# Kernel tuning notes

Hardware: AMD Instinct MI355X
Metric: run time of the kernel (lower is better)

The kernel has to match this reference:

```python
import jax, jax.numpy as jnp
import numpy as np

N_JOINTS = 50
N_BONES = 50  # mask slicing [:, :, :50] / [:, :, :150] in the source requires exactly 50 bones
# Original repo's getSkeletalModelStructure() is not provided; use deterministic
# bone pairs (i, (i+1) % 50) over the 50 joints. Same gather+norm+direction math.
BONE_A = np.arange(N_JOINTS)
BONE_B = (BONE_A + 1) % N_JOINTS


def _length_direct(x):
    # x: [B, T, 150] -> joints [B, T, 50, 3]
    B, T, _ = x.shape
    joints = x.reshape(B, T, N_JOINTS, 3)
    diff = joints[:, :, BONE_A, :] - joints[:, :, BONE_B, :]  # [B, T, 50, 3]
    length = jnp.linalg.norm(diff, axis=-1)                   # [B, T, 50]
    tiny = jnp.finfo(x.dtype).tiny
    direct = diff / (length[..., None] + tiny)                # [B, T, 50, 3]
    return length, direct.reshape(B, T, N_BONES * 3)          # [B, T, 150]


def setup_inputs() -> dict:
    key = jax.random.key(0)
    k1, k2 = jax.random.split(key)
    shape = (128, 1024, 150)
    return {
        "preds": jax.random.normal(k1, shape, dtype=jnp.float32),
        "targets": jax.random.normal(k2, shape, dtype=jnp.float32),
    }


def reference(preds, targets):
    target_pad = 0.0
    loss_scale = 0.1
    mask = (targets != target_pad).astype(preds.dtype)  # [B, T, 150]
    p = preds * mask
    t = targets * mask
    # lengths are computed in the original but unused in the final loss;
    # only the direction terms enter the bone loss.
    _, p_dir = _length_direct(p)
    _, t_dir = _length_direct(t)
    p_dir = p_dir * mask[:, :, :150]
    t_dir = t_dir * mask[:, :, :150]
    loss = jnp.mean(jnp.abs(p - t)) + 0.1 * jnp.mean((p_dir - t_dir) ** 2)
    return loss * loss_scale
```

## Files before the change

kernel.cpp:

```cpp
#include <hip/hip_runtime.h>

constexpr int      FRAMES  = 128 * 1024;
constexpr int      FRAME_F = 150;
constexpr unsigned NT      = (unsigned)FRAMES * 50u;
constexpr unsigned NC      = NT / 4u;
constexpr float    SCALE   = 0.1f / ((float)FRAMES * (float)FRAME_F);

constexpr int      BLOCK   = 256;
constexpr int      NBLK    = 2048;
constexpr unsigned G       = (unsigned)NBLK * BLOCK;

__device__ __forceinline__ float bone_term(
    float p0, float p1, float p2, float t0, float t1, float t2,
    float q0, float q1, float q2, float u0, float u1, float u2)
{
    const float m0 = (t0 != 0.0f) ? 1.0f : 0.0f;
    const float m1 = (t1 != 0.0f) ? 1.0f : 0.0f;
    const float m2 = (t2 != 0.0f) ? 1.0f : 0.0f;
    const float n0 = (u0 != 0.0f) ? 1.0f : 0.0f;
    const float n1 = (u1 != 0.0f) ? 1.0f : 0.0f;
    const float n2 = (u2 != 0.0f) ? 1.0f : 0.0f;

    const float pm0 = p0 * m0, pm1 = p1 * m1, pm2 = p2 * m2;
    const float qm0 = q0 * n0, qm1 = q1 * n1, qm2 = q2 * n2;

    const float ab = fabsf(pm0 - t0) + fabsf(pm1 - t1) + fabsf(pm2 - t2);

    const float pd0 = pm0 - qm0, pd1 = pm1 - qm1, pd2 = pm2 - qm2;
    const float td0 = t0 - u0,   td1 = t1 - u1,   td2 = t2 - u2;

    const float pl2 = pd0*pd0 + pd1*pd1 + pd2*pd2;
    const float tl2 = td0*td0 + td1*td1 + td2*td2;
    const float pri = (pl2 > 0.0f) ? __builtin_amdgcn_rsqf(pl2) : 0.0f;
    const float tri = (tl2 > 0.0f) ? __builtin_amdgcn_rsqf(tl2) : 0.0f;

    const float d0 = pd0 * pri - td0 * tri;
    const float d1 = pd1 * pri - td1 * tri;
    const float d2 = pd2 * pri - td2 * tri;
    const float sq = m0*d0*d0 + m1*d1*d1 + m2*d2*d2;

    return ab + 0.1f * sq;
}

__global__ __launch_bounds__(BLOCK, 4) void bone_loss_main(
    const float* __restrict__ preds,
    const float* __restrict__ targets,
    float* __restrict__ partials)
{
    const unsigned tid = blockIdx.x * BLOCK + threadIdx.x;
    float acc = 0.0f;

    #pragma clang loop unroll(disable)
    for (unsigned c = tid; c < NC; c += G) {
        const unsigned bt = c * 4u;
        const unsigned j0 = bt % 50u;
        const float* P = preds   + (size_t)bt * 3u;
        const float* T = targets + (size_t)bt * 3u;

        const bool w1 = (j0 == 48u);
        const bool w3 = (j0 == 46u);
        const int eoff = w3 ? 0 : 12;
        const int woff = w1 ? -144 : (w3 ? -138 : 0);

        const float4 pa = *reinterpret_cast<const float4*>(P + 0);
        const float4 pb = *reinterpret_cast<const float4*>(P + 4);
        const float4 pc = *reinterpret_cast<const float4*>(P + 8);
        const float4 ps = *reinterpret_cast<const float4*>(P + eoff);
        const float4 ta = *reinterpret_cast<const float4*>(T + 0);
        const float4 tb = *reinterpret_cast<const float4*>(T + 4);
        const float4 tc = *reinterpret_cast<const float4*>(T + 8);
        const float4 ts = *reinterpret_cast<const float4*>(T + eoff);
        const float pw0 = P[woff+0], pw1 = P[woff+1], pw2 = P[woff+2];
        const float tw0 = T[woff+0], tw1 = T[woff+1], tw2 = T[woff+2];

        acc += bone_term(pa.x, pa.y, pa.z,  ta.x, ta.y, ta.z,
                         pa.w, pb.x, pb.y,  ta.w, tb.x, tb.y);
        acc += bone_term(pa.w, pb.x, pb.y,  ta.w, tb.x, tb.y,
                         w1 ? pw0 : pb.z, w1 ? pw1 : pb.w, w1 ? pw2 : pc.x,
                         w1 ? tw0 : tb.z, w1 ? tw1 : tb.w, w1 ? tw2 : tc.x);
        acc += bone_term(pb.z, pb.w, pc.x,  tb.z, tb.w, tc.x,
                         pc.y, pc.z, pc.w,  tc.y, tc.z, tc.w);
        acc += bone_term(pc.y, pc.z, pc.w,  tc.y, tc.z, tc.w,
                         w3 ? pw0 : ps.x, w3 ? pw1 : ps.y, w3 ? pw2 : ps.z,
                         w3 ? tw0 : ts.x, w3 ? tw1 : ts.y, w3 ? tw2 : ts.z);
    }

    #pragma unroll
    for (int off = 32; off > 0; off >>= 1)
        acc += __shfl_down(acc, off, 64);

    __shared__ float ws[4];
    const int wid = threadIdx.x >> 6;
    if ((threadIdx.x & 63) == 0) ws[wid] = acc;
    __syncthreads();
    if (threadIdx.x == 0)
        partials[blockIdx.x] = ws[0] + ws[1] + ws[2] + ws[3];
}

__global__ __launch_bounds__(256) void bone_loss_finish(
    const float* __restrict__ partials,
    float* __restrict__ out)
{
    float v = 0.0f;
    for (int i = threadIdx.x; i < NBLK; i += 256)
        v += partials[i];

    #pragma unroll
    for (int off = 32; off > 0; off >>= 1)
        v += __shfl_down(v, off, 64);

    __shared__ float ws[4];
    const int wid = threadIdx.x >> 6;
    if ((threadIdx.x & 63) == 0) ws[wid] = v;
    __syncthreads();
    if (threadIdx.x == 0)
        out[0] = (ws[0] + ws[1] + ws[2] + ws[3]) * SCALE;
}

extern "C" void kernel_launch(void* const* d_in, const int* in_sizes, int n_in,
                              void* d_out, int out_size, void* d_ws, size_t ws_size,
                              hipStream_t stream) {
    const float* preds   = (const float*)d_in[0];
    const float* targets = (const float*)d_in[1];
    float* out      = (float*)d_out;
    float* partials = (float*)d_ws;

    bone_loss_main<<<NBLK, BLOCK, 0, stream>>>(preds, targets, partials);
    bone_loss_finish<<<1, 256, 0, stream>>>(partials, out);
}
```

Baseline: 175.7 us.

## Fuse final reduction via last-block atomic counter and shuffle neighbor joint loads

```diff
diff --git a/kernel.cpp b/kernel.cpp
--- a/kernel.cpp
+++ b/kernel.cpp
@@ -42,12 +42,10 @@
     return ab + 0.1f * sq;
 }
 
-__global__ __launch_bounds__(BLOCK, 4) void bone_loss_main(
-    const float* __restrict__ preds,
-    const float* __restrict__ targets,
-    float* __restrict__ partials)
+__device__ __forceinline__ float compute_acc(const float* __restrict__ preds,
+                                             const float* __restrict__ targets,
+                                             unsigned tid, int lane)
 {
-    const unsigned tid = blockIdx.x * BLOCK + threadIdx.x;
     float acc = 0.0f;
 
     #pragma clang loop unroll(disable)
@@ -59,19 +57,27 @@
 
         const bool w1 = (j0 == 48u);
         const bool w3 = (j0 == 46u);
-        const int eoff = w3 ? 0 : 12;
         const int woff = w1 ? -144 : (w3 ? -138 : 0);
 
         const float4 pa = *reinterpret_cast<const float4*>(P + 0);
         const float4 pb = *reinterpret_cast<const float4*>(P + 4);
         const float4 pc = *reinterpret_cast<const float4*>(P + 8);
-        const float4 ps = *reinterpret_cast<const float4*>(P + eoff);
         const float4 ta = *reinterpret_cast<const float4*>(T + 0);
         const float4 tb = *reinterpret_cast<const float4*>(T + 4);
         const float4 tc = *reinterpret_cast<const float4*>(T + 8);
-        const float4 ts = *reinterpret_cast<const float4*>(T + eoff);
         const float pw0 = P[woff+0], pw1 = P[woff+1], pw2 = P[woff+2];
         const float tw0 = T[woff+0], tw1 = T[woff+1], tw2 = T[woff+2];
+
+        float sp0 = __shfl_down(pa.x, 1, 64);
+        float sp1 = __shfl_down(pa.y, 1, 64);
+        float sp2 = __shfl_down(pa.z, 1, 64);
+        float st0 = __shfl_down(ta.x, 1, 64);
+        float st1 = __shfl_down(ta.y, 1, 64);
+        float st2 = __shfl_down(ta.z, 1, 64);
+        if (lane == 63 && !w3) {
+            sp0 = P[12]; sp1 = P[13]; sp2 = P[14];
+            st0 = T[12]; st1 = T[13]; st2 = T[14];
+        }
 
         acc += bone_term(pa.x, pa.y, pa.z,  ta.x, ta.y, ta.z,
                          pa.w, pb.x, pb.y,  ta.w, tb.x, tb.y);
@@ -81,9 +87,65 @@
         acc += bone_term(pb.z, pb.w, pc.x,  tb.z, tb.w, tc.x,
                          pc.y, pc.z, pc.w,  tc.y, tc.z, tc.w);
         acc += bone_term(pc.y, pc.z, pc.w,  tc.y, tc.z, tc.w,
-                         w3 ? pw0 : ps.x, w3 ? pw1 : ps.y, w3 ? pw2 : ps.z,
-                         w3 ? tw0 : ts.x, w3 ? tw1 : ts.y, w3 ? tw2 : ts.z);
+                         w3 ? pw0 : sp0, w3 ? pw1 : sp1, w3 ? pw2 : sp2,
+                         w3 ? tw0 : st0, w3 ? tw1 : st1, w3 ? tw2 : st2);
     }
+    return acc;
+}
+
+__global__ __launch_bounds__(BLOCK, 4) void bone_loss_fused(
+    const float* __restrict__ preds,
+    const float* __restrict__ targets,
+    float* __restrict__ partials,
+    unsigned* __restrict__ counter,
+    float* __restrict__ out)
+{
+    const unsigned tid = blockIdx.x * BLOCK + threadIdx.x;
+    const int lane = threadIdx.x & 63;
+
+    float acc = compute_acc(preds, targets, tid, lane);
+
+    #pragma unroll
+    for (int off = 32; off > 0; off >>= 1)
+        acc += __shfl_down(acc, off, 64);
+
+    __shared__ float ws[4];
+    __shared__ unsigned sdone;
+    const int wid = threadIdx.x >> 6;
+    if (lane == 0) ws[wid] = acc;
+    __syncthreads();
+
+    if (threadIdx.x == 0) {
+        partials[blockIdx.x] = ws[0] + ws[1] + ws[2] + ws[3];
+        __threadfence();
+        const unsigned old = atomicAdd(counter, 1u);
+        sdone = (old == (unsigned)NBLK - 1u) ? 1u : 0u;
+    }
+    __syncthreads();
+
+    if (sdone) {
+        __threadfence();
+        float v = 0.0f;
+        for (int i = threadIdx.x; i < NBLK; i += BLOCK)
+            v += partials[i];
+        #pragma unroll
+        for (int off = 32; off > 0; off >>= 1)
+            v += __shfl_down(v, off, 64);
+        if (lane == 0) ws[wid] = v;
+        __syncthreads();
+        if (threadIdx.x == 0)
+            out[0] = (ws[0] + ws[1] + ws[2] + ws[3]) * SCALE;
+    }
+}
+
+__global__ __launch_bounds__(BLOCK, 4) void bone_loss_main(
+    const float* __restrict__ preds,
+    const float* __restrict__ targets,
+    float* __restrict__ partials)
+{
+    const unsigned tid = blockIdx.x * BLOCK + threadIdx.x;
+    const int lane = threadIdx.x & 63;
+    float acc = compute_acc(preds, targets, tid, lane);
 
     #pragma unroll
     for (int off = 32; off > 0; off >>= 1)
@@ -91,7 +153,7 @@
 
     __shared__ float ws[4];
     const int wid = threadIdx.x >> 6;
-    if ((threadIdx.x & 63) == 0) ws[wid] = acc;
+    if (lane == 0) ws[wid] = acc;
     __syncthreads();
     if (threadIdx.x == 0)
         partials[blockIdx.x] = ws[0] + ws[1] + ws[2] + ws[3];
@@ -125,6 +187,13 @@
     float* out      = (float*)d_out;
     float* partials = (float*)d_ws;
 
-    bone_loss_main<<<NBLK, BLOCK, 0, stream>>>(preds, targets, partials);
-    bone_loss_finish<<<1, 256, 0, stream>>>(partials, out);
+    if (ws_size >= (size_t)NBLK * 4 + 4) {
+        unsigned* counter = (unsigned*)((char*)d_ws + (size_t)NBLK * 4);
+        hipMemsetAsync(counter, 0, 4, stream);
+        bone_loss_fused<<<NBLK, BLOCK, 0, stream>>>(preds, targets, partials,
+                                                    counter, out);
+    } else {
+        bone_loss_main<<<NBLK, BLOCK, 0, stream>>>(preds, targets, partials);
+        bone_loss_finish<<<1, 256, 0, stream>>>(partials, out);
+    }
 }
```

Result: slower. 276.5 us (+57.4%).
